# Kernel tuning notes

Hardware: AMD Instinct MI355X
Metric: run time of the kernel (lower is better)

Reference implementation:

```python
import jax, jax.numpy as jnp
import numpy as np

B, N, L, D, H = 8, 128, 4096, 1024, 16

def setup_inputs() -> dict:
    key = jax.random.key(0)
    ks = jax.random.split(key, 7)
    s = 1.0 / np.sqrt(D)  # xavier-ish scale for square D x D weights
    return {
        "q": jax.random.normal(ks[0], (B, N, D), dtype=jnp.float32),
        "k": jax.random.normal(ks[1], (B, L, D), dtype=jnp.float32),
        "v": jax.random.normal(ks[2], (B, L, D), dtype=jnp.float32),
        "Wq": jax.random.normal(ks[3], (D, D), dtype=jnp.float32) * s,
        "Wk": jax.random.normal(ks[4], (D, D), dtype=jnp.float32) * s,
        "Wv": jax.random.normal(ks[5], (D, D), dtype=jnp.float32) * s,
        "Wo": jax.random.normal(ks[6], (D, D), dtype=jnp.float32) * s,
    }

def reference(q, k, v, Wq, Wk, Wv, Wo):
    Bq, Nq, Dm = q.shape
    Lk = k.shape[1]
    Hh = H
    Dh = Dm // Hh
    scale = Dm ** (-0.5)  # note: scaled by d_model, not head_dim (faithful to source)
    # projections (nn.Linear with weight (out,in): y = x @ W.T)
    qh = (q @ Wq.T).reshape(Bq, Nq, Hh, Dh).transpose(0, 2, 1, 3)  # B H N Dh
    kh = (k @ Wk.T).reshape(Bq, Lk, Hh, Dh).transpose(0, 2, 1, 3)  # B H L Dh
    vh = (v @ Wv.T).reshape(Bq, Lk, Hh, Dh).transpose(0, 2, 1, 3)  # B H L Dh
    attn = jnp.einsum('bhnc,bhlc->bhnl', qh * scale, kh)          # B H N L
    # inverted attention: softmax over the query (N) axis...
    attn = jax.nn.softmax(attn, axis=2)
    # ...then L1-renormalize over the key (L) axis
    attn = attn / jnp.sum(attn, axis=-1, keepdims=True)
    out = jnp.einsum('bhnl,bhlc->bhnc', attn, vh)                 # B H N Dh
    out = out.transpose(0, 2, 1, 3).reshape(Bq, Nq, Dm)
    return out @ Wo.T
```

## Files before the change

### kernel.cpp

```cpp
#include <hip/hip_runtime.h>
#include <stdint.h>

typedef __bf16 bf16_t;
typedef __bf16 bf16x4 __attribute__((ext_vector_type(4)));
typedef __bf16 bf16x8 __attribute__((ext_vector_type(8)));
typedef float f32x4 __attribute__((ext_vector_type(4)));
typedef unsigned int u32;

constexpr int CB = 8, CN = 128, CL = 4096, CD = 1024, CH = 16, CDh = 64;

__device__ __forceinline__ bf16x4 cvt4(float4 v) {
  bf16x4 r;
  r[0] = (__bf16)v.x; r[1] = (__bf16)v.y; r[2] = (__bf16)v.z; r[3] = (__bf16)v.w;
  return r;
}
__device__ __forceinline__ bf16x8 cvt8v(f32x4 lo, f32x4 hi) {
  bf16x8 r;
#pragma unroll
  for (int i = 0; i < 4; ++i) { r[i] = (__bf16)lo[i]; r[i + 4] = (__bf16)hi[i]; }
  return r;
}

__device__ __forceinline__ void async16(void* lds, const void* g) {
  __builtin_amdgcn_global_load_lds(
      (const __attribute__((address_space(1))) u32*)g,
      (__attribute__((address_space(3))) u32*)lds, 16, 0, 0);
}

__global__ __launch_bounds__(256) void cvt_f32_bf16(const float* __restrict__ in,
                                                    bf16_t* __restrict__ outp, int n4) {
  int i = (int)blockIdx.x * 256 + (int)threadIdx.x;
  if (i < n4) {
    float4 v = reinterpret_cast<const float4*>(in)[i];
    reinterpret_cast<bf16x4*>(outp)[i] = cvt4(v);
  }
}

template<bool AF32, bool CF32>
__global__ __launch_bounds__(256)
void gemm_dma(const void* __restrict__ Ap, const bf16_t* __restrict__ Bw,
              void* __restrict__ Cp, int mblocks, int N, int K) {
  constexpr int ASZ = AF32 ? 16384 : 8192;
  __shared__ __attribute__((aligned(16))) char AsB[2][ASZ];
  __shared__ __attribute__((aligned(16))) char BsB[2][8192];

  const int t = (int)threadIdx.x;
  const int lane = t & 63, wv = t >> 6;
  const int bid = (int)blockIdx.x;
  const int x = bid & 7;
  const int j = bid >> 3;
  const int S = mblocks >> 3;
  const int mb = (S > 0) ? (x * S + (j >> 3)) : (j >> 3);
  const int nb = j & 7;
  const int brow = mb * 128;
  const int bcol = nb * 128;
  const int wm = (wv >> 1) * 64, wn = (wv & 1) * 64;
  const int fr = lane & 15, fq = lane >> 4;

  const float*  Af = (const float*)Ap;
  const bf16_t* Ab = (const bf16_t*)Ap;

  auto stageA = [&](char* dst, int k0) {
    if constexpr (AF32) {
      const int r8 = lane >> 3, u = lane & 7;
#pragma unroll
      for (int i = 0; i < 4; ++i) {
        const int seg = i * 4 + wv;
        const int row = seg * 8 + r8;
        const int col = ((u ^ (row & 7)) << 2);
        async16(dst + seg * 1024, Af + (size_t)(brow + row) * K + k0 + col);
      }
    } else {
      const int r4 = lane >> 2, u = lane & 3;
#pragma unroll
      for (int i = 0; i < 2; ++i) {
        const int seg = i * 4 + wv;
        const int row = seg * 16 + r4;
        const int col = ((u ^ ((row >> 1) & 3)) << 3);
        async16(dst + seg * 1024, Ab + (size_t)(brow + row) * K + k0 + col);
      }
    }
  };
  auto stageB = [&](char* dst, int k0) {
    const int r4 = lane >> 2, u = lane & 3;
#pragma unroll
    for (int i = 0; i < 2; ++i) {
      const int seg = i * 4 + wv;
      const int row = seg * 16 + r4;
      const int col = ((u ^ ((row >> 1) & 3)) << 3);
      async16(dst + seg * 1024, Bw + (size_t)(bcol + row) * K + k0 + col);
    }
  };

  const f32x4 z = {0.f, 0.f, 0.f, 0.f};
  f32x4 acc[4][4];
#pragma unroll
  for (int m = 0; m < 4; ++m)
#pragma unroll
    for (int n = 0; n < 4; ++n) acc[m][n] = z;

  const int nt = K >> 5;
  stageA(AsB[0], 0);
  stageB(BsB[0], 0);
  __syncthreads();
  int cur = 0;

  for (int tt = 0; tt < nt; ++tt) {
    if (tt + 1 < nt) {
      stageA(AsB[cur ^ 1], (tt + 1) << 5);
      stageB(BsB[cur ^ 1], (tt + 1) << 5);
    }
    const char* Ac = AsB[cur];
    const char* Bc = BsB[cur];

    bf16x8 af[4], bfg[4];
#pragma unroll
    for (int m = 0; m < 4; ++m) {
      const int R = wm + m * 16 + fr;
      if constexpr (AF32) {
        const int xx = (R & 7) << 4;
        const f32x4 lo = *(const f32x4*)(Ac + R * 128 + ((fq << 5) ^ xx));
        const f32x4 hi = *(const f32x4*)(Ac + R * 128 + (((fq << 5) + 16) ^ xx));
        af[m] = cvt8v(lo, hi);
      } else {
        const int ph = (fq << 4) ^ (((R >> 1) & 3) << 4);
        af[m] = *(const bf16x8*)(Ac + R * 64 + ph);
      }
    }
#pragma unroll
    for (int n = 0; n < 4; ++n) {
      const int R = wn + n * 16 + fr;
      const int ph = (fq << 4) ^ (((R >> 1) & 3) << 4);
      bfg[n] = *(const bf16x8*)(Bc + R * 64 + ph);
    }
#pragma unroll
    for (int m = 0; m < 4; ++m)
#pragma unroll
      for (int n = 0; n < 4; ++n)
        acc[m][n] = __builtin_amdgcn_mfma_f32_16x16x32_bf16(af[m], bfg[n], acc[m][n], 0, 0, 0);

    __syncthreads();
    cur ^= 1;
  }

  const int rb = fq * 4;
#pragma unroll
  for (int m = 0; m < 4; ++m)
#pragma unroll
    for (int n = 0; n < 4; ++n)
#pragma unroll
      for (int r = 0; r < 4; ++r) {
        const int row = brow + wm + m * 16 + rb + r;
        const int col = bcol + wn + n * 16 + fr;
        if constexpr (CF32)
          ((float*)Cp)[(size_t)row * N + col] = acc[m][n][r];
        else
          ((bf16_t*)Cp)[(size_t)row * N + col] = (__bf16)acc[m][n][r];
      }
}

template<bool A_IS_F32, bool C_IS_F32>
__global__ __launch_bounds__(256)
void gemm_bt(const void* __restrict__ Ap, const float* __restrict__ Bw,
             void* __restrict__ Cp, int M, int N, int K) {
  (void)M;
  __shared__ bf16_t As[128][40];
  __shared__ bf16_t Bs[128][40];
  const int t = (int)threadIdx.x;
  const int lane = t & 63, wv = t >> 6;
  const int wm = (wv >> 1) * 64, wn = (wv & 1) * 64;
  const int brow = (int)blockIdx.y * 128, bcol = (int)blockIdx.x * 128;
  const int fr = lane & 15, fk = (lane >> 4) * 8;

  const f32x4 z = {0.f, 0.f, 0.f, 0.f};
  f32x4 acc[4][4];
#pragma unroll
  for (int m = 0; m < 4; ++m)
#pragma unroll
    for (int n = 0; n < 4; ++n) acc[m][n] = z;

  for (int k0 = 0; k0 < K; k0 += 32) {
    if constexpr (A_IS_F32) {
      const float* A = (const float*)Ap;
      const int tr = t >> 3, tc = (t & 7) * 4;
#pragma unroll
      for (int p = 0; p < 4; ++p) {
        const int r = p * 32 + tr;
        float4 v = *reinterpret_cast<const float4*>(A + (size_t)(brow + r) * K + k0 + tc);
        *reinterpret_cast<bf16x4*>(&As[r][tc]) = cvt4(v);
      }
    } else {
      const bf16_t* A = (const bf16_t*)Ap;
      const int tr = t >> 2, tc = (t & 3) * 8;
#pragma unroll
      for (int p = 0; p < 2; ++p) {
        const int r = p * 64 + tr;
        *reinterpret_cast<int4*>(&As[r][tc]) =
            *reinterpret_cast<const int4*>(A + (size_t)(brow + r) * K + k0 + tc);
      }
    }
    {
      const int tr = t >> 3, tc = (t & 7) * 4;
#pragma unroll
      for (int p = 0; p < 4; ++p) {
        const int r = p * 32 + tr;
        float4 v = *reinterpret_cast<const float4*>(Bw + (size_t)(bcol + r) * K + k0 + tc);
        *reinterpret_cast<bf16x4*>(&Bs[r][tc]) = cvt4(v);
      }
    }
    __syncthreads();
    bf16x8 af[4], bfr[4];
#pragma unroll
    for (int m = 0; m < 4; ++m)
      af[m] = *reinterpret_cast<const bf16x8*>(&As[wm + m * 16 + fr][fk]);
#pragma unroll
    for (int n = 0; n < 4; ++n)
      bfr[n] = *reinterpret_cast<const bf16x8*>(&Bs[wn + n * 16 + fr][fk]);
#pragma unroll
    for (int m = 0; m < 4; ++m)
#pragma unroll
      for (int n = 0; n < 4; ++n)
        acc[m][n] = __builtin_amdgcn_mfma_f32_16x16x32_bf16(af[m], bfr[n], acc[m][n], 0, 0, 0);
    __syncthreads();
  }
  const int rb = (lane >> 4) * 4;
#pragma unroll
  for (int m = 0; m < 4; ++m)
#pragma unroll
    for (int n = 0; n < 4; ++n)
#pragma unroll
      for (int r = 0; r < 4; ++r) {
        const int row = brow + wm + m * 16 + rb + r;
        const int col = bcol + wn + n * 16 + fr;
        if constexpr (C_IS_F32)
          ((float*)Cp)[(size_t)row * N + col] = acc[m][n][r];
        else
          ((bf16_t*)Cp)[(size_t)row * N + col] = (__bf16)acc[m][n][r];
      }
}

template<bool DIRECT>
__global__ __launch_bounds__(256)
void attn_inv(const bf16_t* __restrict__ qh, const bf16_t* __restrict__ kh,
              const bf16_t* __restrict__ vh, bf16_t* __restrict__ ao,
              float* __restrict__ part, int lcount) {
  const int bh = (int)blockIdx.x;
  const int b = bh >> 4, h = bh & 15;
  const int l_begin = (int)blockIdx.y * lcount;

  __shared__ bf16_t Qs[128][72];
  __shared__ bf16_t Ks[64][72];
  __shared__ bf16_t Vt[80][72];
  __shared__ bf16_t Ps[128][72];

  const int t = (int)threadIdx.x;
  const int lane = t & 63, w = t >> 6;
  const int fr = lane & 15, fq = lane >> 4;

  const bf16_t* qb = qh + (size_t)(b * CN) * CD + h * CDh;
#pragma unroll
  for (int p = 0; p < 4; ++p) {
    const int j = p * 256 + t;
    const int r = j >> 3, cc = (j & 7) * 8;
    *reinterpret_cast<int4*>(&Qs[r][cc]) =
        *reinterpret_cast<const int4*>(qb + (size_t)r * CD + cc);
  }
#pragma unroll
  for (int p = 0; p < 4; ++p) {
    const int j = p * 256 + t;
    const int r = 64 + (j >> 6), c = j & 63;
    Vt[r][c] = (r == 64) ? (__bf16)1.0f : (__bf16)0.0f;
  }

  const f32x4 z = {0.f, 0.f, 0.f, 0.f};
  f32x4 acc[2][5];
#pragma unroll
  for (int m = 0; m < 2; ++m)
#pragma unroll
    for (int n = 0; n < 5; ++n) acc[m][n] = z;

  for (int l0 = l_begin; l0 < l_begin + lcount; l0 += 64) {
    __syncthreads();
    const bf16_t* kb = kh + (size_t)(b * CL + l0) * CD + h * CDh;
    const bf16_t* vb = vh + (size_t)(b * CL + l0) * CD + h * CDh;
#pragma unroll
    for (int p = 0; p < 2; ++p) {
      const int j = p * 256 + t;
      const int r = j >> 3, cc = (j & 7) * 8;
      *reinterpret_cast<int4*>(&Ks[r][cc]) =
          *reinterpret_cast<const int4*>(kb + (size_t)r * CD + cc);
      int4 vv = *reinterpret_cast<const int4*>(vb + (size_t)r * CD + cc);
      const bf16_t* hp = reinterpret_cast<const bf16_t*>(&vv);
#pragma unroll
      for (int i = 0; i < 8; ++i) Vt[cc + i][r] = hp[i];
    }
    __syncthreads();

    f32x4 s[8];
#pragma unroll
    for (int m = 0; m < 8; ++m) s[m] = z;
#pragma unroll
    for (int ks = 0; ks < 2; ++ks) {
      bf16x8 bk = *reinterpret_cast<const bf16x8*>(&Ks[w * 16 + fr][ks * 32 + fq * 8]);
#pragma unroll
      for (int m = 0; m < 8; ++m) {
        bf16x8 aq = *reinterpret_cast<const bf16x8*>(&Qs[m * 16 + fr][ks * 32 + fq * 8]);
        s[m] = __builtin_amdgcn_mfma_f32_16x16x32_bf16(aq, bk, s[m], 0, 0, 0);
      }
    }

    float p[8][4];
    float mx = -3.0e38f;
#pragma unroll
    for (int m = 0; m < 8; ++m)
#pragma unroll
      for (int r = 0; r < 4; ++r) {
        const float x = s[m][r] * 0.03125f;
        p[m][r] = x;
        mx = fmaxf(mx, x);
      }
    mx = fmaxf(mx, __shfl_xor(mx, 16));
    mx = fmaxf(mx, __shfl_xor(mx, 32));
    float sum = 0.f;
#pragma unroll
    for (int m = 0; m < 8; ++m)
#pragma unroll
      for (int r = 0; r < 4; ++r) {
        const float e = __expf(p[m][r] - mx);
        p[m][r] = e;
        sum += e;
      }
    sum += __shfl_xor(sum, 16);
    sum += __shfl_xor(sum, 32);
    const float inv = 1.0f / sum;
    const int pcol = w * 16 + fr;
#pragma unroll
    for (int m = 0; m < 8; ++m)
#pragma unroll
      for (int r = 0; r < 4; ++r)
        Ps[m * 16 + fq * 4 + r][pcol] = (__bf16)(p[m][r] * inv);
    __syncthreads();

#pragma unroll
    for (int ks = 0; ks < 2; ++ks) {
      bf16x8 pa[2];
#pragma unroll
      for (int m = 0; m < 2; ++m)
        pa[m] = *reinterpret_cast<const bf16x8*>(&Ps[w * 32 + m * 16 + fr][ks * 32 + fq * 8]);
#pragma unroll
      for (int n = 0; n < 5; ++n) {
        bf16x8 bv = *reinterpret_cast<const bf16x8*>(&Vt[n * 16 + fr][ks * 32 + fq * 8]);
#pragma unroll
        for (int m = 0; m < 2; ++m)
          acc[m][n] = __builtin_amdgcn_mfma_f32_16x16x32_bf16(pa[m], bv, acc[m][n], 0, 0, 0);
      }
    }
  }

  if constexpr (DIRECT) {
    bf16_t* ob = ao + (size_t)(b * CN) * CD + h * CDh;
#pragma unroll
    for (int m = 0; m < 2; ++m)
#pragma unroll
      for (int r = 0; r < 4; ++r) {
        const float R = __shfl(acc[m][4][r], lane & 48);
        const float invr = 1.0f / R;
        const int row = w * 32 + m * 16 + fq * 4 + r;
#pragma unroll
        for (int n = 0; n < 4; ++n) {
          const int col = n * 16 + fr;
          ob[(size_t)row * CD + col] = (__bf16)(acc[m][n][r] * invr);
        }
      }
  } else {
    float* pb = part + ((size_t)blockIdx.y * (CB * CH) + bh) * (size_t)(CN * 72);
#pragma unroll
    for (int m = 0; m < 2; ++m)
#pragma unroll
      for (int r = 0; r < 4; ++r) {
        const int row = w * 32 + m * 16 + fq * 4 + r;
#pragma unroll
        for (int n = 0; n < 4; ++n)
          pb[(size_t)row * 72 + n * 16 + fr] = acc[m][n][r];
        if (fr == 0) pb[(size_t)row * 72 + 64] = acc[m][4][r];
      }
  }
}

__global__ __launch_bounds__(256)
void attn_reduce(const float* __restrict__ part, bf16_t* __restrict__ ao, int nsplit) {
  const int idx = (int)blockIdx.x * 256 + (int)threadIdx.x;
  const int c = idx & 63;
  const int n = (idx >> 6) & 127;
  const int bh = idx >> 13;
  const float* p = part + (size_t)bh * (CN * 72) + (size_t)n * 72;
  const size_t sstr = (size_t)(CB * CH) * (CN * 72);
  float o = 0.f, r = 0.f;
  for (int s = 0; s < nsplit; ++s) {
    o += p[(size_t)s * sstr + c];
    r += p[(size_t)s * sstr + 64];
  }
  const int b = bh >> 4, h = bh & 15;
  ao[((size_t)(b * CN + n)) * CD + h * CDh + c] = (__bf16)(o / r);
}

extern "C" void kernel_launch(void* const* d_in, const int* in_sizes, int n_in,
                              void* d_out, int out_size, void* d_ws, size_t ws_size,
                              hipStream_t stream) {
  (void)in_sizes; (void)n_in; (void)out_size;
  const float* q  = (const float*)d_in[0];
  const float* k  = (const float*)d_in[1];
  const float* v  = (const float*)d_in[2];
  const float* Wq = (const float*)d_in[3];
  const float* Wk = (const float*)d_in[4];
  const float* Wv = (const float*)d_in[5];
  const float* Wo = (const float*)d_in[6];
  float* out = (float*)d_out;

  const size_t MiB = (size_t)1 << 20;
  const size_t QH_OFF = 0;
  const size_t KH_OFF = 2 * MiB;
  const size_t VH_OFF = KH_OFF + 64 * MiB;
  const size_t AO_OFF = VH_OFF + 64 * MiB;
  const size_t FIXED  = AO_OFF + 2 * MiB;
  if (ws_size < FIXED) return;

  char* ws = (char*)d_ws;
  bf16_t* qh = (bf16_t*)(ws + QH_OFF);
  bf16_t* kh = (bf16_t*)(ws + KH_OFF);
  bf16_t* vh = (bf16_t*)(ws + VH_OFF);
  bf16_t* ao = (bf16_t*)(ws + AO_OFF);

  const int M_q = CB * CN;
  const int M_kv = CB * CL;
  const int W4 = CD * CD / 4;
  const int A4_kv = M_kv * CD / 4;
  const int A4_q  = M_q * CD / 4;

  const size_t WBUF_OFF = FIXED;
  const size_t QC_OFF   = WBUF_OFF + 2 * MiB;
  const size_t KC_OFF   = QC_OFF + 2 * MiB;
  const size_t NEED_FAST = KC_OFF + 64 * MiB;

  const size_t PB = (size_t)CB * CH * CN * 72 * 4;

  if (ws_size >= NEED_FAST) {
    bf16_t* wbuf = (bf16_t*)(ws + WBUF_OFF);
    bf16_t* qc   = (bf16_t*)(ws + QC_OFF);
    bf16_t* kc   = (bf16_t*)(ws + KC_OFF);
    float*  part = (float*)(ws + KC_OFF);

    cvt_f32_bf16<<<A4_q / 256, 256, 0, stream>>>(q, qc, A4_q);
    cvt_f32_bf16<<<W4 / 256, 256, 0, stream>>>(Wq, wbuf, W4);
    gemm_dma<false, false><<<(M_q / 128) * 8, 256, 0, stream>>>(qc, wbuf, qh, M_q / 128, CD, CD);

    cvt_f32_bf16<<<A4_kv / 256, 256, 0, stream>>>(k, kc, A4_kv);
    cvt_f32_bf16<<<W4 / 256, 256, 0, stream>>>(Wk, wbuf, W4);
    gemm_dma<false, false><<<(M_kv / 128) * 8, 256, 0, stream>>>(kc, wbuf, kh, M_kv / 128, CD, CD);

    cvt_f32_bf16<<<A4_kv / 256, 256, 0, stream>>>(v, kc, A4_kv);
    cvt_f32_bf16<<<W4 / 256, 256, 0, stream>>>(Wv, wbuf, W4);
    gemm_dma<false, false><<<(M_kv / 128) * 8, 256, 0, stream>>>(kc, wbuf, vh, M_kv / 128, CD, CD);

    attn_inv<false><<<dim3(CB * CH, 8), 256, 0, stream>>>(qh, kh, vh, ao, part, CL / 8);
    attn_reduce<<<(CB * CH * CN * 64) / 256, 256, 0, stream>>>(part, ao, 8);

    cvt_f32_bf16<<<W4 / 256, 256, 0, stream>>>(Wo, wbuf, W4);
    gemm_dma<false, true><<<(M_q / 128) * 8, 256, 0, stream>>>(ao, wbuf, out, M_q / 128, CD, CD);
    return;
  }

  const size_t extra = ws_size - FIXED;
  const bool newgemm = extra >= 2 * MiB;
  bf16_t* wbuf = (bf16_t*)(ws + FIXED);
  const size_t pav = newgemm ? (extra - 2 * MiB) : 0;
  int nsplit = 8;
  while (nsplit > 1 && (size_t)nsplit * PB > pav) nsplit >>= 1;
  float* part = (float*)(ws + FIXED + 2 * MiB);

  if (newgemm) {
    cvt_f32_bf16<<<W4 / 256, 256, 0, stream>>>(Wq, wbuf, W4);
    gemm_dma<true, false><<<(M_q / 128) * 8, 256, 0, stream>>>(q, wbuf, qh, M_q / 128, CD, CD);
    cvt_f32_bf16<<<W4 / 256, 256, 0, stream>>>(Wk, wbuf, W4);
    gemm_dma<true, false><<<(M_kv / 128) * 8, 256, 0, stream>>>(k, wbuf, kh, M_kv / 128, CD, CD);
    cvt_f32_bf16<<<W4 / 256, 256, 0, stream>>>(Wv, wbuf, W4);
    gemm_dma<true, false><<<(M_kv / 128) * 8, 256, 0, stream>>>(v, wbuf, vh, M_kv / 128, CD, CD);
  } else {
    gemm_bt<true, false><<<dim3(CD / 128, M_q / 128),  256, 0, stream>>>(q, Wq, qh, M_q,  CD, CD);
    gemm_bt<true, false><<<dim3(CD / 128, M_kv / 128), 256, 0, stream>>>(k, Wk, kh, M_kv, CD, CD);
    gemm_bt<true, false><<<dim3(CD / 128, M_kv / 128), 256, 0, stream>>>(v, Wv, vh, M_kv, CD, CD);
  }

  if (nsplit > 1) {
    attn_inv<false><<<dim3(CB * CH, nsplit), 256, 0, stream>>>(qh, kh, vh, ao, part, CL / nsplit);
    attn_reduce<<<(CB * CH * CN * 64) / 256, 256, 0, stream>>>(part, ao, nsplit);
  } else {
    attn_inv<true><<<dim3(CB * CH, 1), 256, 0, stream>>>(qh, kh, vh, ao, nullptr, CL);
  }

  if (newgemm) {
    cvt_f32_bf16<<<W4 / 256, 256, 0, stream>>>(Wo, wbuf, W4);
    gemm_dma<false, true><<<(M_q / 128) * 8, 256, 0, stream>>>(ao, wbuf, out, M_q / 128, CD, CD);
  } else {
    gemm_bt<false, true><<<dim3(CD / 128, M_q / 128), 256, 0, stream>>>(ao, Wo, out, M_q, CD, CD);
  }
}
```

Measured before the change: 368.7 us.

## Add 256x256-tile 8-wave pipelined GEMM for K and V projections

Introduces gemm8, a 512-thread kernel with 256x256 output tiles and K-step 64. It uses a two-deep async global-to-LDS prefetch with XOR swizzle, interleaves LDS reads, prefetch and MFMA phases separated by explicit barriers, and raises MFMA priority with setprio. The large K/V projection GEMMs switch to it to raise data reuse per LDS byte and overlap loads with compute. The fallback path is simplified and the unused fp32-A variant of gemm_dma is removed. The cost is 128KB of LDS per block and a heavy register load, which risks lower occupancy and spills.

```diff
diff --git a/kernel.cpp b/kernel.cpp
--- a/kernel.cpp
+++ b/kernel.cpp
@@ -9,15 +9,16 @@
 
 constexpr int CB = 8, CN = 128, CL = 4096, CD = 1024, CH = 16, CDh = 64;
 
+#define BAR()                                    \
+  do {                                           \
+    __asm__ volatile("" ::: "memory");           \
+    __builtin_amdgcn_s_barrier();                \
+    __asm__ volatile("" ::: "memory");           \
+  } while (0)
+
 __device__ __forceinline__ bf16x4 cvt4(float4 v) {
   bf16x4 r;
   r[0] = (__bf16)v.x; r[1] = (__bf16)v.y; r[2] = (__bf16)v.z; r[3] = (__bf16)v.w;
-  return r;
-}
-__device__ __forceinline__ bf16x8 cvt8v(f32x4 lo, f32x4 hi) {
-  bf16x8 r;
-#pragma unroll
-  for (int i = 0; i < 4; ++i) { r[i] = (__bf16)lo[i]; r[i + 4] = (__bf16)hi[i]; }
   return r;
 }
 
@@ -36,12 +37,142 @@
   }
 }
 
-template<bool AF32, bool CF32>
+__global__ __launch_bounds__(512, 2)
+void gemm8(const bf16_t* __restrict__ A, const bf16_t* __restrict__ Bw,
+           bf16_t* __restrict__ C, int mblocks, int N, int K) {
+  __shared__ __attribute__((aligned(16))) char lds[131072];
+
+  const int t = (int)threadIdx.x;
+  const int lane = t & 63, w = t >> 6;
+  const int wave_m = w >> 2, wave_n = w & 3;
+  const int fr = lane & 15, fq = lane >> 4;
+  const int bid = (int)blockIdx.x;
+  const int x = bid & 7, j = bid >> 3;
+  const int S = mblocks >> 3;
+  const int nnb = N >> 8;
+  const int mb = x * S + (j / nnb);
+  const int nb = j % nnb;
+  const int brow = mb * 256, bcol = nb * 256;
+
+  auto Aoff = [](int buf, int half) { return (buf * 2 + half) * 16384; };
+  auto Boff = [](int buf, int half) { return 65536 + (buf * 2 + half) * 16384; };
+
+  auto stage = [&](int tile, bool dA, bool dB) {
+    const int buf = tile & 1;
+    const int k0 = tile << 6;
+#pragma unroll
+    for (int n = 0; n < 2; ++n) {
+      const int idx = n * 512 + t;
+      const int row = idx >> 3;
+      const int u = (idx & 7) ^ (row & 7);
+      const int dst = (n * 8 + w) * 1024;
+      if (dB) {
+#pragma unroll
+        for (int h = 0; h < 2; ++h)
+          async16(lds + Boff(buf, h) + dst,
+                  Bw + (size_t)(bcol + h * 128 + row) * K + k0 + u * 8);
+      }
+      if (dA) {
+#pragma unroll
+        for (int h = 0; h < 2; ++h)
+          async16(lds + Aoff(buf, h) + dst,
+                  A + (size_t)(brow + h * 128 + row) * K + k0 + u * 8);
+      }
+    }
+  };
+
+  bf16x8 af[4][2], blo[2][2], bhi[2][2];
+  auto rdA = [&](int buf, int mq) {
+    const char* base = lds + Aoff(buf, wave_m);
+#pragma unroll
+    for (int mf = 0; mf < 4; ++mf) {
+      const int row = mq * 64 + mf * 16 + fr;
+#pragma unroll
+      for (int ks = 0; ks < 2; ++ks)
+        af[mf][ks] = *(const bf16x8*)(base + row * 128 + (((ks * 4 + fq) ^ (row & 7)) << 4));
+    }
+  };
+  auto rdB = [&](bf16x8 (&bf)[2][2], int buf, int nq) {
+    const char* base = lds + Boff(buf, wave_n >> 1);
+#pragma unroll
+    for (int nf = 0; nf < 2; ++nf) {
+      const int row = (wave_n & 1) * 64 + (nq * 2 + nf) * 16 + fr;
+#pragma unroll
+      for (int ks = 0; ks < 2; ++ks)
+        bf[nf][ks] = *(const bf16x8*)(base + row * 128 + (((ks * 4 + fq) ^ (row & 7)) << 4));
+    }
+  };
+
+  const f32x4 z = {0.f, 0.f, 0.f, 0.f};
+  f32x4 acc[8][4];
+#pragma unroll
+  for (int m = 0; m < 8; ++m)
+#pragma unroll
+    for (int n = 0; n < 4; ++n) acc[m][n] = z;
+
+  auto mma = [&](const bf16x8 (&bf)[2][2], int mq, int nq) {
+    __builtin_amdgcn_s_setprio(1);
+#pragma unroll
+    for (int mf = 0; mf < 4; ++mf)
+#pragma unroll
+      for (int nf = 0; nf < 2; ++nf)
+#pragma unroll
+        for (int ks = 0; ks < 2; ++ks)
+          acc[mq * 4 + mf][nq * 2 + nf] = __builtin_amdgcn_mfma_f32_16x16x32_bf16(
+              af[mf][ks], bf[nf][ks], acc[mq * 4 + mf][nq * 2 + nf], 0, 0, 0);
+    __builtin_amdgcn_s_setprio(0);
+  };
+
+  const int nt = K >> 6;
+  stage(0, true, true);
+  stage(1, true, true);
+  asm volatile("s_waitcnt vmcnt(8)" ::: "memory");
+  BAR();
+
+  for (int i = 0; i < nt; ++i) {
+    const int buf = i & 1;
+    rdA(buf, 0);
+    rdB(blo, buf, 0);
+    BAR();
+    mma(blo, 0, 0);
+    BAR();
+    rdB(bhi, buf, 1);
+    BAR();
+    mma(bhi, 0, 1);
+    BAR();
+    rdA(buf, 1);
+    if (i + 2 < nt) stage(i + 2, false, true);
+    BAR();
+    mma(blo, 1, 0);
+    BAR();
+    if (i + 2 < nt) stage(i + 2, true, false);
+    if (i == nt - 2) {
+      asm volatile("s_waitcnt vmcnt(0)" ::: "memory");
+    } else if (i < nt - 2) {
+      asm volatile("s_waitcnt vmcnt(8)" ::: "memory");
+    }
+    BAR();
+    mma(bhi, 1, 1);
+    BAR();
+  }
+
+#pragma unroll
+  for (int mf = 0; mf < 8; ++mf)
+#pragma unroll
+    for (int nf = 0; nf < 4; ++nf)
+#pragma unroll
+      for (int r = 0; r < 4; ++r) {
+        const int row = brow + wave_m * 128 + mf * 16 + fq * 4 + r;
+        const int col = bcol + wave_n * 64 + nf * 16 + fr;
+        C[(size_t)row * N + col] = (__bf16)acc[mf][nf][r];
+      }
+}
+
+template<bool CF32>
 __global__ __launch_bounds__(256)
-void gemm_dma(const void* __restrict__ Ap, const bf16_t* __restrict__ Bw,
+void gemm_dma(const bf16_t* __restrict__ Ab, const bf16_t* __restrict__ Bw,
               void* __restrict__ Cp, int mblocks, int N, int K) {
-  constexpr int ASZ = AF32 ? 16384 : 8192;
-  __shared__ __attribute__((aligned(16))) char AsB[2][ASZ];
+  __shared__ __attribute__((aligned(16))) char AsB[2][8192];
   __shared__ __attribute__((aligned(16))) char BsB[2][8192];
 
   const int t = (int)threadIdx.x;
@@ -57,38 +188,14 @@
   const int wm = (wv >> 1) * 64, wn = (wv & 1) * 64;
   const int fr = lane & 15, fq = lane >> 4;
 
-  const float*  Af = (const float*)Ap;
-  const bf16_t* Ab = (const bf16_t*)Ap;
-
-  auto stageA = [&](char* dst, int k0) {
-    if constexpr (AF32) {
-      const int r8 = lane >> 3, u = lane & 7;
-#pragma unroll
-      for (int i = 0; i < 4; ++i) {
-        const int seg = i * 4 + wv;
-        const int row = seg * 8 + r8;
-        const int col = ((u ^ (row & 7)) << 2);
-        async16(dst + seg * 1024, Af + (size_t)(brow + row) * K + k0 + col);
-      }
-    } else {
-      const int r4 = lane >> 2, u = lane & 3;
-#pragma unroll
-      for (int i = 0; i < 2; ++i) {
-        const int seg = i * 4 + wv;
-        const int row = seg * 16 + r4;
-        const int col = ((u ^ ((row >> 1) & 3)) << 3);
-        async16(dst + seg * 1024, Ab + (size_t)(brow + row) * K + k0 + col);
-      }
-    }
-  };
-  auto stageB = [&](char* dst, int k0) {
+  auto stageT = [&](char* dst, const bf16_t* src, int rbase, int k0) {
     const int r4 = lane >> 2, u = lane & 3;
 #pragma unroll
     for (int i = 0; i < 2; ++i) {
       const int seg = i * 4 + wv;
       const int row = seg * 16 + r4;
       const int col = ((u ^ ((row >> 1) & 3)) << 3);
-      async16(dst + seg * 1024, Bw + (size_t)(bcol + row) * K + k0 + col);
+      async16(dst + seg * 1024, src + (size_t)(rbase + row) * K + k0 + col);
     }
   };
 
@@ -100,15 +207,15 @@
     for (int n = 0; n < 4; ++n) acc[m][n] = z;
 
   const int nt = K >> 5;
-  stageA(AsB[0], 0);
-  stageB(BsB[0], 0);
+  stageT(AsB[0], Ab, brow, 0);
+  stageT(BsB[0], Bw, bcol, 0);
   __syncthreads();
   int cur = 0;
 
   for (int tt = 0; tt < nt; ++tt) {
     if (tt + 1 < nt) {
-      stageA(AsB[cur ^ 1], (tt + 1) << 5);
-      stageB(BsB[cur ^ 1], (tt + 1) << 5);
+      stageT(AsB[cur ^ 1], Ab, brow, (tt + 1) << 5);
+      stageT(BsB[cur ^ 1], Bw, bcol, (tt + 1) << 5);
     }
     const char* Ac = AsB[cur];
     const char* Bc = BsB[cur];
@@ -117,15 +224,8 @@
 #pragma unroll
     for (int m = 0; m < 4; ++m) {
       const int R = wm + m * 16 + fr;
-      if constexpr (AF32) {
-        const int xx = (R & 7) << 4;
-        const f32x4 lo = *(const f32x4*)(Ac + R * 128 + ((fq << 5) ^ xx));
-        const f32x4 hi = *(const f32x4*)(Ac + R * 128 + (((fq << 5) + 16) ^ xx));
-        af[m] = cvt8v(lo, hi);
-      } else {
-        const int ph = (fq << 4) ^ (((R >> 1) & 3) << 4);
-        af[m] = *(const bf16x8*)(Ac + R * 64 + ph);
-      }
+      const int ph = (fq << 4) ^ (((R >> 1) & 3) << 4);
+      af[m] = *(const bf16x8*)(Ac + R * 64 + ph);
     }
 #pragma unroll
     for (int n = 0; n < 4; ++n) {
@@ -315,9 +415,9 @@
     for (int m = 0; m < 8; ++m)
 #pragma unroll
       for (int r = 0; r < 4; ++r) {
-        const float x = s[m][r] * 0.03125f;
-        p[m][r] = x;
-        mx = fmaxf(mx, x);
+        const float xv = s[m][r] * 0.03125f;
+        p[m][r] = xv;
+        mx = fmaxf(mx, xv);
       }
     mx = fmaxf(mx, __shfl_xor(mx, 16));
     mx = fmaxf(mx, __shfl_xor(mx, 32));
@@ -442,8 +542,6 @@
   const size_t KC_OFF   = QC_OFF + 2 * MiB;
   const size_t NEED_FAST = KC_OFF + 64 * MiB;
 
-  const size_t PB = (size_t)CB * CH * CN * 72 * 4;
-
   if (ws_size >= NEED_FAST) {
     bf16_t* wbuf = (bf16_t*)(ws + WBUF_OFF);
     bf16_t* qc   = (bf16_t*)(ws + QC_OFF);
@@ -452,56 +550,27 @@
 
     cvt_f32_bf16<<<A4_q / 256, 256, 0, stream>>>(q, qc, A4_q);
     cvt_f32_bf16<<<W4 / 256, 256, 0, stream>>>(Wq, wbuf, W4);
-    gemm_dma<false, false><<<(M_q / 128) * 8, 256, 0, stream>>>(qc, wbuf, qh, M_q / 128, CD, CD);
+    gemm_dma<false><<<(M_q / 128) * 8, 256, 0, stream>>>(qc, wbuf, qh, M_q / 128, CD, CD);
 
     cvt_f32_bf16<<<A4_kv / 256, 256, 0, stream>>>(k, kc, A4_kv);
     cvt_f32_bf16<<<W4 / 256, 256, 0, stream>>>(Wk, wbuf, W4);
-    gemm_dma<false, false><<<(M_kv / 128) * 8, 256, 0, stream>>>(kc, wbuf, kh, M_kv / 128, CD, CD);
+    gemm8<<<(M_kv / 256) * (CD / 256), 512, 0, stream>>>(kc, wbuf, kh, M_kv / 256, CD, CD);
 
     cvt_f32_bf16<<<A4_kv / 256, 256, 0, stream>>>(v, kc, A4_kv);
     cvt_f32_bf16<<<W4 / 256, 256, 0, stream>>>(Wv, wbuf, W4);
-    gemm_dma<false, false><<<(M_kv / 128) * 8, 256, 0, stream>>>(kc, wbuf, vh, M_kv / 128, CD, CD);
+    gemm8<<<(M_kv / 256) * (CD / 256), 512, 0, stream>>>(kc, wbuf, vh, M_kv / 256, CD, CD);
 
     attn_inv<false><<<dim3(CB * CH, 8), 256, 0, stream>>>(qh, kh, vh, ao, part, CL / 8);
     attn_reduce<<<(CB * CH * CN * 64) / 256, 256, 0, stream>>>(part, ao, 8);
 
     cvt_f32_bf16<<<W4 / 256, 256, 0, stream>>>(Wo, wbuf, W4);
-    gemm_dma<false, true><<<(M_q / 128) * 8, 256, 0, stream>>>(ao, wbuf, out, M_q / 128, CD, CD);
+    gemm_dma<true><<<(M_q / 128) * 8, 256, 0, stream>>>(ao, wbuf, out, M_q / 128, CD, CD);
     return;
   }
 
-  const size_t extra = ws_size - FIXED;
-  const bool newgemm = extra >= 2 * MiB;
-  bf16_t* wbuf = (bf16_t*)(ws + FIXED);
-  const size_t pav = newgemm ? (extra - 2 * MiB) : 0;
-  int nsplit = 8;
-  while (nsplit > 1 && (size_t)nsplit * PB > pav) nsplit >>= 1;
-  float* part = (float*)(ws + FIXED + 2 * MiB);
-
-  if (newgemm) {
-    cvt_f32_bf16<<<W4 / 256, 256, 0, stream>>>(Wq, wbuf, W4);
-    gemm_dma<true, false><<<(M_q / 128) * 8, 256, 0, stream>>>(q, wbuf, qh, M_q / 128, CD, CD);
-    cvt_f32_bf16<<<W4 / 256, 256, 0, stream>>>(Wk, wbuf, W4);
-    gemm_dma<true, false><<<(M_kv / 128) * 8, 256, 0, stream>>>(k, wbuf, kh, M_kv / 128, CD, CD);
-    cvt_f32_bf16<<<W4 / 256, 256, 0, stream>>>(Wv, wbuf, W4);
-    gemm_dma<true, false><<<(M_kv / 128) * 8, 256, 0, stream>>>(v, wbuf, vh, M_kv / 128, CD, CD);
-  } else {
-    gemm_bt<true, false><<<dim3(CD / 128, M_q / 128),  256, 0, stream>>>(q, Wq, qh, M_q,  CD, CD);
-    gemm_bt<true, false><<<dim3(CD / 128, M_kv / 128), 256, 0, stream>>>(k, Wk, kh, M_kv, CD, CD);
-    gemm_bt<true, false><<<dim3(CD / 128, M_kv / 128), 256, 0, stream>>>(v, Wv, vh, M_kv, CD, CD);
-  }
-
-  if (nsplit > 1) {
-    attn_inv<false><<<dim3(CB * CH, nsplit), 256, 0, stream>>>(qh, kh, vh, ao, part, CL / nsplit);
-    attn_reduce<<<(CB * CH * CN * 64) / 256, 256, 0, stream>>>(part, ao, nsplit);
-  } else {
-    attn_inv<true><<<dim3(CB * CH, 1), 256, 0, stream>>>(qh, kh, vh, ao, nullptr, CL);
-  }
-
-  if (newgemm) {
-    cvt_f32_bf16<<<W4 / 256, 256, 0, stream>>>(Wo, wbuf, W4);
-    gemm_dma<false, true><<<(M_q / 128) * 8, 256, 0, stream>>>(ao, wbuf, out, M_q / 128, CD, CD);
-  } else {
-    gemm_bt<false, true><<<dim3(CD / 128, M_q / 128), 256, 0, stream>>>(ao, Wo, out, M_q, CD, CD);
-  }
-}
+  gemm_bt<true, false><<<dim3(CD / 128, M_q / 128),  256, 0, stream>>>(q, Wq, qh, M_q,  CD, CD);
+  gemm_bt<true, false><<<dim3(CD / 128, M_kv / 128), 256, 0, stream>>>(k, Wk, kh, M_kv, CD, CD);
+  gemm_bt<true, false><<<dim3(CD / 128, M_kv / 128), 256, 0, stream>>>(v, Wv, vh, M_kv, CD, CD);
+  attn_inv<true><<<dim3(CB * CH, 1), 256, 0, stream>>>(qh, kh, vh, ao, nullptr, CL);
+  gemm_bt<false, true><<<dim3(CD / 128, M_q / 128), 256, 0, stream>>>(ao, Wo, out, M_q, CD, CD);
+}
```

New measurement: 340.2 us. -7.7%, faster.
